# Kernel tuning notes

Hardware: AMD Instinct MI355X
Metric: run time of the kernel (lower is better)

Reference implementation:

```python
import jax, jax.numpy as jnp
import numpy as np
import math

N_SRC = 100000
N_DST0 = 30000
N_DST1 = 8000
E0 = 200000
E1 = 80000
H, D = 4, 64


def gat_conv(h_src, h_dst, src, dst, W, al, ar, b, n_dst):
    """DGL GATConv (allow_zero_in_degree=True): shared fc, LeakyReLU(0.2), edge softmax."""
    z_src = (h_src @ W).reshape(-1, H, D)              # [Ns,H,D]
    z_dst = (h_dst @ W).reshape(-1, H, D)              # [Nd,H,D]
    el = jnp.sum(z_src * al, axis=-1)                  # [Ns,H]
    er = jnp.sum(z_dst * ar, axis=-1)                  # [Nd,H]
    e = jax.nn.leaky_relu(el[src] + er[dst], 0.2)      # [E,H]
    emax = jax.ops.segment_max(e, dst, num_segments=n_dst)
    emax = jnp.where(jnp.isfinite(emax), emax, 0.0)
    ex = jnp.exp(e - emax[dst])
    denom = jax.ops.segment_sum(ex, dst, num_segments=n_dst)
    denom = jnp.where(denom > 0, denom, 1.0)
    alpha = ex / denom[dst]                            # [E,H]
    out = jax.ops.segment_sum(alpha[:, :, None] * z_src[src], dst, num_segments=n_dst)
    return out + b.reshape(1, H, D)                    # [Nd,H,D]


def attn_pool(feat):
    """Self attention over relation/head slots, then mean over slots (attention(f,f,f).mean(dim=1))."""
    d = feat.shape[-1]
    scores = jnp.einsum('nsd,ntd->nst', feat, feat) / math.sqrt(d)
    p = jax.nn.softmax(scores, axis=-1)
    out = jnp.einsum('nst,ntd->nsd', p, feat)
    return out.mean(axis=1)                            # [N,d]


def rgat_layer(xu, xi, eii, eiu, eui, W, al, ar, b, n_dst_u, n_dst_i):
    du, di = xu[:n_dst_u], xi[:n_dst_i]
    # sorted canonical etypes: ('item','ii','item') < ('item','iu','user') < ('user','ui','item')
    out_ii = gat_conv(xi, di, eii[0], eii[1], W[0], al[0], ar[0], b[0], n_dst_i)
    out_iu = gat_conv(xi, du, eiu[0], eiu[1], W[1], al[1], ar[1], b[1], n_dst_u)
    out_ui = gat_conv(xu, di, eui[0], eui[1], W[2], al[2], ar[2], b[2], n_dst_i)
    feat_u = out_iu                                    # [Nu, H, D]
    feat_i = jnp.concatenate([out_ii, out_ui], axis=1) # [Ni, 2H, D]
    hu = attn_pool(feat_u)
    hi = attn_pool(feat_i)
    return jnp.concatenate([du, hu], axis=1), jnp.concatenate([di, hi], axis=1)


def setup_inputs() -> dict:
    key = jax.random.key(0)
    ks = jax.random.split(key, 24)
    inp = {
        'x_user': jax.random.normal(ks[0], (N_SRC, 64), jnp.float32),
        'x_item': jax.random.normal(ks[1], (N_SRC, 64), jnp.float32),
        'e0_ii_src': jax.random.randint(ks[2], (E0,), 0, N_SRC, jnp.int32),
        'e0_ii_dst': jax.random.randint(ks[3], (E0,), 0, N_DST0, jnp.int32),
        'e0_iu_src': jax.random.randint(ks[4], (E0,), 0, N_SRC, jnp.int32),
        'e0_iu_dst': jax.random.randint(ks[5], (E0,), 0, N_DST0, jnp.int32),
        'e0_ui_src': jax.random.randint(ks[6], (E0,), 0, N_SRC, jnp.int32),
        'e0_ui_dst': jax.random.randint(ks[7], (E0,), 0, N_DST0, jnp.int32),
        'e1_ii_src': jax.random.randint(ks[8], (E1,), 0, N_DST0, jnp.int32),
        'e1_ii_dst': jax.random.randint(ks[9], (E1,), 0, N_DST1, jnp.int32),
        'e1_iu_src': jax.random.randint(ks[10], (E1,), 0, N_DST0, jnp.int32),
        'e1_iu_dst': jax.random.randint(ks[11], (E1,), 0, N_DST1, jnp.int32),
        'e1_ui_src': jax.random.randint(ks[12], (E1,), 0, N_DST0, jnp.int32),
        'e1_ui_dst': jax.random.randint(ks[13], (E1,), 0, N_DST1, jnp.int32),
        'W0': jax.random.normal(ks[14], (3, 64, H * D), jnp.float32) * 0.1,
        'al0': jax.random.normal(ks[15], (3, H, D), jnp.float32) * 0.1,
        'ar0': jax.random.normal(ks[16], (3, H, D), jnp.float32) * 0.1,
        'b0': jnp.zeros((3, H * D), jnp.float32),
        'W1': jax.random.normal(ks[17], (3, 128, H * D), jnp.float32) * 0.1,
        'al1': jax.random.normal(ks[18], (3, H, D), jnp.float32) * 0.1,
        'ar1': jax.random.normal(ks[19], (3, H, D), jnp.float32) * 0.1,
        'b1': jnp.zeros((3, H * D), jnp.float32),
    }
    return inp


def reference(x_user, x_item,
              e0_ii_src, e0_ii_dst, e0_iu_src, e0_iu_dst, e0_ui_src, e0_ui_dst,
              e1_ii_src, e1_ii_dst, e1_iu_src, e1_iu_dst, e1_ui_src, e1_ui_dst,
              W0, al0, ar0, b0, W1, al1, ar1, b1):
    xu, xi = rgat_layer(x_user, x_item,
                        (e0_ii_src, e0_ii_dst), (e0_iu_src, e0_iu_dst), (e0_ui_src, e0_ui_dst),
                        W0, al0, ar0, b0, N_DST0, N_DST0)
    xu, xi = rgat_layer(xu, xi,
                        (e1_ii_src, e1_ii_dst), (e1_iu_src, e1_iu_dst), (e1_ui_src, e1_ui_dst),
                        W1, al1, ar1, b1, N_DST1, N_DST1)
    return jnp.concatenate([xu, xi], axis=0)  # [2*N_DST1, 128+64]
```

## Files before the change

### kernel.cpp

```cpp
#include <hip/hip_runtime.h>

#define NSRC   100000
#define NDST0  30000
#define NDST1  8000
#define E0N    200000
#define E1N    80000
#define HD     256
#define DD     64
#define CAP    64

typedef short bf16x8 __attribute__((ext_vector_type(8)));
typedef float f32x4  __attribute__((ext_vector_type(4)));

static __device__ __forceinline__ unsigned short f2bf(float f) {
    unsigned u = __float_as_uint(f);
    u += 0x7fffu + ((u >> 16) & 1u);
    return (unsigned short)(u >> 16);
}
static __device__ __forceinline__ unsigned pack2(float a, float b) {
    return (unsigned)f2bf(a) | ((unsigned)f2bf(b) << 16);
}
static __device__ __forceinline__ void fma4(float4& a, float s, const float4& b) {
    a.x = fmaf(s, b.x, a.x); a.y = fmaf(s, b.y, a.y);
    a.z = fmaf(s, b.z, a.z); a.w = fmaf(s, b.w, a.w);
}
static __device__ __forceinline__ float dot4(const float4& a, const float4& b) {
    return fmaf(a.x, b.x, fmaf(a.y, b.y, fmaf(a.z, b.z, a.w * b.w)));
}
static __device__ __forceinline__ float4 ld_bf4(const unsigned short* p) {
    uint2 u = *reinterpret_cast<const uint2*>(p);
    float4 r;
    r.x = __uint_as_float(u.x << 16);
    r.y = __uint_as_float(u.x & 0xffff0000u);
    r.z = __uint_as_float(u.y << 16);
    r.w = __uint_as_float(u.y & 0xffff0000u);
    return r;
}
static __device__ __forceinline__ void red4(float4& a, int m) {
    a.x += __shfl_xor(a.x, m, 64);
    a.y += __shfl_xor(a.y, m, 64);
    a.z += __shfl_xor(a.z, m, 64);
    a.w += __shfl_xor(a.w, m, 64);
}

template<int K>
__global__ void k_wprep(const float* __restrict__ W, const float* __restrict__ al,
                        const float* __restrict__ ar, float* __restrict__ wl,
                        float* __restrict__ wr, unsigned short* __restrict__ Wt)
{
    constexpr int WLRB = (3 * K * 4) / 256;
    int bx = blockIdx.x;
    if (bx < WLRB) {
        int tid = bx * 256 + threadIdx.x;
        int r = tid / (K * 4);
        int rem = tid - r * K * 4;
        int k = rem >> 2, h = rem & 3;
        const float* wrow = W + (size_t)r * K * HD + (size_t)k * HD + h * DD;
        const float* a_l = al + r * HD + h * DD;
        const float* a_r = ar + r * HD + h * DD;
        float sl = 0.f, sr = 0.f;
        for (int d = 0; d < DD; ++d) {
            float w = wrow[d];
            sl = fmaf(w, a_l[d], sl);
            sr = fmaf(w, a_r[d], sr);
        }
        wl[r * 512 + k * 4 + h] = sl;
        wr[r * 512 + k * 4 + h] = sr;
    } else {
        int r = bx - WLRB;
        const float* Wr = W + (size_t)r * K * HD;
        unsigned short* Wtr = Wt + (size_t)r * 256 * K;
        int c = threadIdx.x;
        #pragma unroll 4
        for (int k = 0; k < K; k += 2) {
            float a = Wr[(size_t)k * HD + c];
            float b = Wr[(size_t)(k + 1) * HD + c];
            *reinterpret_cast<unsigned*>(Wtr + (size_t)c * K + k) = pack2(a, b);
        }
    }
}

template<int K, bool MIRROR>
__global__ __launch_bounds__(256) void k_prep_x2(const float* __restrict__ XA,
                                                 const float* __restrict__ XB,
                                                 int M, int nd, int bpr,
                                                 const float* __restrict__ wl3,
                                                 const float* __restrict__ wr3,
                                                 float* __restrict__ el3,
                                                 float* __restrict__ er3,
                                                 unsigned short* __restrict__ XbA,
                                                 unsigned short* __restrict__ XbB)
{
    int bx = blockIdx.x;
    const bool item = bx < bpr;
    int row = (item ? bx : bx - bpr) * 256 + threadIdx.x;
    if (row >= M) return;
    const float* X = item ? XA : XB;
    const float4* xv = reinterpret_cast<const float4*>(X + (size_t)row * K);

    if (MIRROR) {
        unsigned short* xbrow = (item ? XbA : XbB) + (size_t)row * K;
        #pragma unroll
        for (int c2 = 0; c2 < K / 8; ++c2) {
            float4 a = xv[2 * c2], b = xv[2 * c2 + 1];
            uint4 w;
            w.x = pack2(a.x, a.y); w.y = pack2(a.z, a.w);
            w.z = pack2(b.x, b.y); w.w = pack2(b.z, b.w);
            reinterpret_cast<uint4*>(xbrow)[c2] = w;
        }
    }

    const float4* wlAv = reinterpret_cast<const float4*>(item ? wl3 : wl3 + 1024);
    const float4* wlBv = reinterpret_cast<const float4*>(wl3 + 512);
    float4 aA = make_float4(0.f, 0.f, 0.f, 0.f), aB = aA;
    #pragma unroll
    for (int c = 0; c < K / 4; ++c) {
        float4 x4 = xv[c];
        fma4(aA, x4.x, wlAv[c * 4 + 0]); fma4(aA, x4.y, wlAv[c * 4 + 1]);
        fma4(aA, x4.z, wlAv[c * 4 + 2]); fma4(aA, x4.w, wlAv[c * 4 + 3]);
        if (item) {
            fma4(aB, x4.x, wlBv[c * 4 + 0]); fma4(aB, x4.y, wlBv[c * 4 + 1]);
            fma4(aB, x4.z, wlBv[c * 4 + 2]); fma4(aB, x4.w, wlBv[c * 4 + 3]);
        }
    }
    if (item) {
        *reinterpret_cast<float4*>(el3 + (size_t)row * 4) = aA;
        *reinterpret_cast<float4*>(el3 + (size_t)NSRC * 4 + (size_t)row * 4) = aB;
    } else {
        *reinterpret_cast<float4*>(el3 + (size_t)2 * NSRC * 4 + (size_t)row * 4) = aA;
    }
    if (row < nd) {
        const float4* wrAv = reinterpret_cast<const float4*>(item ? wr3 : wr3 + 512);
        const float4* wrBv = reinterpret_cast<const float4*>(wr3 + 1024);
        float4 rA = make_float4(0.f, 0.f, 0.f, 0.f), rB = rA;
        #pragma unroll
        for (int c = 0; c < K / 4; ++c) {
            float4 x4 = xv[c];
            fma4(rA, x4.x, wrAv[c * 4 + 0]); fma4(rA, x4.y, wrAv[c * 4 + 1]);
            fma4(rA, x4.z, wrAv[c * 4 + 2]); fma4(rA, x4.w, wrAv[c * 4 + 3]);
            if (item) {
                fma4(rB, x4.x, wrBv[c * 4 + 0]); fma4(rB, x4.y, wrBv[c * 4 + 1]);
                fma4(rB, x4.z, wrBv[c * 4 + 2]); fma4(rB, x4.w, wrBv[c * 4 + 3]);
            }
        }
        if (item) {
            *reinterpret_cast<float4*>(er3 + (size_t)row * 4) = rA;
            *reinterpret_cast<float4*>(er3 + (size_t)2 * NDST0 * 4 + (size_t)row * 4) = rB;
        } else {
            *reinterpret_cast<float4*>(er3 + (size_t)NDST0 * 4 + (size_t)row * 4) = rA;
        }
    }
}

__global__ void k_fill3(const int* __restrict__ ed0, const int* __restrict__ ed1,
                        const int* __restrict__ ed2, const int* __restrict__ es0,
                        const int* __restrict__ es1, const int* __restrict__ es2,
                        int* __restrict__ cnt, int* __restrict__ bsrc,
                        int E, int nd, int bpr)
{
    int bx = blockIdx.x;
    int r = (bx >= 2 * bpr) ? 2 : (bx >= bpr ? 1 : 0);
    int e = (bx - r * bpr) * 256 + threadIdx.x;
    if (e >= E) return;
    const int* ed = (r == 0) ? ed0 : (r == 1 ? ed1 : ed2);
    const int* es = (r == 0) ? es0 : (r == 1 ? es1 : es2);
    int d = ed[e];
    int c = atomicAdd(&cnt[(size_t)r * nd + d], 1);
    if (c < CAP) bsrc[((size_t)r * nd + d) * CAP + c] = es[e];
}

template<int K>
__global__ __launch_bounds__(256) void k_agg3(const int* __restrict__ cnt,
                                              const int* __restrict__ bsrc,
                                              const float* __restrict__ el3,
                                              const float* __restrict__ er3,
                                              const unsigned short* __restrict__ xsA,
                                              const unsigned short* __restrict__ xsB,
                                              unsigned short* __restrict__ aggX,
                                              int nd, int bpr)
{
    constexpr int NV = K / 64;
    int bx = blockIdx.x;
    int r = (bx >= 2 * bpr) ? 2 : (bx >= bpr ? 1 : 0);
    int wid = ((bx - r * bpr) * 256 + (int)threadIdx.x) >> 6;
    int lane = threadIdx.x & 63;
    if (wid >= nd) return;
    int q = lane & 15, g = lane >> 4;
    const float* el = el3 + (size_t)r * NSRC * 4;
    const unsigned short* xsrc = (r < 2) ? xsA : xsB;
    int c = cnt[(size_t)r * nd + wid]; if (c > CAP) c = CAP;
    const int* lst = bsrc + ((size_t)r * nd + wid) * CAP;
    float4 er4 = *reinterpret_cast<const float4*>(er3 + (size_t)r * NDST0 * 4 + (size_t)wid * 4);

    int s_own = 0;
    float4 ex_own = make_float4(0.f, 0.f, 0.f, 0.f);
    if (lane < c) {
        s_own = lst[lane];
        float4 e4 = *reinterpret_cast<const float4*>(el + (size_t)s_own * 4);
        e4.x += er4.x; e4.y += er4.y; e4.z += er4.z; e4.w += er4.w;
        e4.x = e4.x > 0.f ? e4.x : 0.2f * e4.x;
        e4.y = e4.y > 0.f ? e4.y : 0.2f * e4.y;
        e4.z = e4.z > 0.f ? e4.z : 0.2f * e4.z;
        e4.w = e4.w > 0.f ? e4.w : 0.2f * e4.w;
        ex_own.x = __expf(e4.x); ex_own.y = __expf(e4.y);
        ex_own.z = __expf(e4.z); ex_own.w = __expf(e4.w);
    }

    float4 acc[4][NV];
    #pragma unroll
    for (int h = 0; h < 4; ++h)
        #pragma unroll
        for (int v = 0; v < NV; ++v) acc[h][v] = make_float4(0.f, 0.f, 0.f, 0.f);
    float4 den = make_float4(0.f, 0.f, 0.f, 0.f);

    const int nt = (c + 3) >> 2;
    for (int t = 0; t < nt; ++t) {
        int i = g + 4 * t;
        int ilane = i & 63;
        int   s   = __shfl(s_own,    ilane, 64);
        float ex0 = __shfl(ex_own.x, ilane, 64);
        float ex1 = __shfl(ex_own.y, ilane, 64);
        float ex2 = __shfl(ex_own.z, ilane, 64);
        float ex3 = __shfl(ex_own.w, ilane, 64);
        if (i < c) {
            const unsigned short* xp = xsrc + (size_t)s * K + q * 4 * NV;
            #pragma unroll
            for (int v = 0; v < NV; ++v) {
                float4 x4 = ld_bf4(xp + v * 4);
                fma4(acc[0][v], ex0, x4);
                fma4(acc[1][v], ex1, x4);
                fma4(acc[2][v], ex2, x4);
                fma4(acc[3][v], ex3, x4);
            }
            den.x += ex0; den.y += ex1; den.z += ex2; den.w += ex3;
        }
    }
    #pragma unroll
    for (int m = 16; m < 64; m <<= 1) {
        #pragma unroll
        for (int h = 0; h < 4; ++h)
            #pragma unroll
            for (int v = 0; v < NV; ++v) red4(acc[h][v], m);
        red4(den, m);
    }
    float invh[4];
    invh[0] = den.x > 0.f ? 1.f / den.x : 0.f;
    invh[1] = den.y > 0.f ? 1.f / den.y : 0.f;
    invh[2] = den.z > 0.f ? 1.f / den.z : 0.f;
    invh[3] = den.w > 0.f ? 1.f / den.w : 0.f;
    #pragma unroll
    for (int h = 0; h < 4; ++h) {
        unsigned short* op = aggX + ((size_t)r * nd * 4 + (size_t)wid * 4 + h) * K + q * 4 * NV;
        if (NV == 1) {
            uint2 w;
            w.x = pack2(acc[h][0].x * invh[h], acc[h][0].y * invh[h]);
            w.y = pack2(acc[h][0].z * invh[h], acc[h][0].w * invh[h]);
            *reinterpret_cast<uint2*>(op) = w;
        } else {
            uint4 w;
            w.x = pack2(acc[h][0].x * invh[h], acc[h][0].y * invh[h]);
            w.y = pack2(acc[h][0].z * invh[h], acc[h][0].w * invh[h]);
            w.z = pack2(acc[h][1].x * invh[h], acc[h][1].y * invh[h]);
            w.w = pack2(acc[h][1].z * invh[h], acc[h][1].w * invh[h]);
            *reinterpret_cast<uint4*>(op) = w;
        }
    }
}

template<int K>
__global__ __launch_bounds__(256) void k_gemm3(const unsigned short* __restrict__ aggX,
                                               const unsigned short* __restrict__ Wt3,
                                               unsigned short* __restrict__ outb,
                                               int nd, int bpr)
{
    int bx = blockIdx.x;
    int r = (bx >= 2 * bpr) ? 2 : (bx >= bpr ? 1 : 0);
    const unsigned short* A  = aggX + (size_t)r * nd * 4 * K;
    const unsigned short* Wt = Wt3 + (size_t)r * 256 * K;
    unsigned short* ob = outb + (size_t)r * NDST0 * HD;
    const int lane = threadIdx.x & 63;
    const int wv = threadIdx.x >> 6;
    const int r0 = (bx - r * bpr) * 16;
    const int rr = lane & 15, kg = lane >> 4;
    f32x4 acc[4] = {{0.f,0.f,0.f,0.f},{0.f,0.f,0.f,0.f},{0.f,0.f,0.f,0.f},{0.f,0.f,0.f,0.f}};
    const unsigned short* ap = A + ((size_t)(r0 + rr) * 4 + wv) * K + kg * 8;
    #pragma unroll
    for (int kb = 0; kb < K; kb += 32) {
        bf16x8 a = *reinterpret_cast<const bf16x8*>(ap + kb);
        #pragma unroll
        for (int n = 0; n < 4; ++n) {
            const unsigned short* wp = Wt + (size_t)(wv * 64 + n * 16 + rr) * K + kb + kg * 8;
            bf16x8 b = *reinterpret_cast<const bf16x8*>(wp);
            acc[n] = __builtin_amdgcn_mfma_f32_16x16x32_bf16(a, b, acc[n], 0, 0, 0);
        }
    }
    #pragma unroll
    for (int n = 0; n < 4; ++n)
        #pragma unroll
        for (int i = 0; i < 4; ++i)
            ob[(size_t)(r0 + kg * 4 + i) * HD + wv * 64 + n * 16 + rr] = f2bf(acc[n][i]);
}

template<int S>
__global__ __launch_bounds__(256) void k_pool2(const unsigned short* __restrict__ srcA, const float* __restrict__ bA,
                                               const unsigned short* __restrict__ srcB, const float* __restrict__ bB,
                                               const float* __restrict__ base, int baseCols,
                                               float* __restrict__ dst, int pitch, int colOff, int n)
{
    int wid = (blockIdx.x * 256 + threadIdx.x) >> 6;
    int lane = threadIdx.x & 63;
    int node = wid * 4 + (lane >> 4);
    int q = lane & 15;
    if (node >= n) return;

    float4 f[S];
    #pragma unroll
    for (int s = 0; s < S; ++s) {
        const unsigned short* sp = (s < 4) ? (srcA + (size_t)node * HD + s * DD)
                                           : (srcB + (size_t)node * HD + (s - 4) * DD);
        const float* bp = (s < 4) ? (bA + s * DD) : (bB + (s - 4) * DD);
        float4 v = ld_bf4(sp + q * 4);
        float4 b = *reinterpret_cast<const float4*>(bp + q * 4);
        v.x += b.x; v.y += b.y; v.z += b.z; v.w += b.w;
        f[s] = v;
    }
    constexpr int NE = S * (S + 1) / 2;
    float gt[NE];
    {
        int idx = 0;
        #pragma unroll
        for (int s = 0; s < S; ++s)
            #pragma unroll
            for (int t = s; t < S; ++t)
                gt[idx++] = dot4(f[s], f[t]);
    }
    #pragma unroll
    for (int m = 1; m < 16; m <<= 1) {
        #pragma unroll
        for (int i = 0; i < NE; ++i) gt[i] += __shfl_xor(gt[i], m, 16);
    }
    auto Gv = [&](int s, int t) -> float {
        int a = s < t ? s : t, b2 = s < t ? t : s;
        return gt[a * S - a * (a - 1) / 2 + (b2 - a)];
    };
    float g[S];
    #pragma unroll
    for (int t = 0; t < S; ++t) g[t] = 0.f;
    #pragma unroll
    for (int s = 0; s < S; ++s) {
        float sc[S];
        float m = -1e30f;
        #pragma unroll
        for (int t = 0; t < S; ++t) { sc[t] = Gv(s, t) * 0.125f; m = sc[t] > m ? sc[t] : m; }
        float pe[S];
        float sum = 0.f;
        #pragma unroll
        for (int t = 0; t < S; ++t) { pe[t] = __expf(sc[t] - m); sum += pe[t]; }
        float inv = 1.f / sum;
        #pragma unroll
        for (int t = 0; t < S; ++t) g[t] += pe[t] * inv;
    }
    float4 o = make_float4(0.f, 0.f, 0.f, 0.f);
    #pragma unroll
    for (int t = 0; t < S; ++t) fma4(o, g[t], f[t]);
    const float is = 1.f / S;
    o.x *= is; o.y *= is; o.z *= is; o.w *= is;
    *reinterpret_cast<float4*>(dst + (size_t)node * pitch + colOff + q * 4) = o;
    for (int c = q * 4; c < baseCols; c += 64) {
        float4 v = *reinterpret_cast<const float4*>(base + (size_t)node * baseCols + c);
        *reinterpret_cast<float4*>(dst + (size_t)node * pitch + c) = v;
    }
}

extern "C" void kernel_launch(void* const* d_in, const int* in_sizes, int n_in,
                              void* d_out, int out_size, void* d_ws, size_t ws_size,
                              hipStream_t stream)
{
    const float* x_user = (const float*)d_in[0];
    const float* x_item = (const float*)d_in[1];
    const int* e_s[6] = { (const int*)d_in[2], (const int*)d_in[4], (const int*)d_in[6],
                          (const int*)d_in[8], (const int*)d_in[10], (const int*)d_in[12] };
    const int* e_d[6] = { (const int*)d_in[3], (const int*)d_in[5], (const int*)d_in[7],
                          (const int*)d_in[9], (const int*)d_in[11], (const int*)d_in[13] };
    const float* W0  = (const float*)d_in[14];
    const float* al0 = (const float*)d_in[15];
    const float* ar0 = (const float*)d_in[16];
    const float* b0  = (const float*)d_in[17];
    const float* W1  = (const float*)d_in[18];
    const float* al1 = (const float*)d_in[19];
    const float* ar1 = (const float*)d_in[20];
    const float* b1  = (const float*)d_in[21];
    float* out = (float*)d_out;
    (void)in_sizes; (void)n_in; (void)out_size; (void)ws_size;

    char* p = (char*)d_ws;
    auto take = [&](size_t bytes) { char* r = p; p += (bytes + 255) & ~(size_t)255; return r; };
    unsigned short* out3 = (unsigned short*)take((size_t)3 * NDST0 * HD * 2);
    float* xu1  = (float*)take((size_t)NDST0 * 128 * 4);
    float* xi1  = (float*)take((size_t)NDST0 * 128 * 4);
    unsigned short* xib  = (unsigned short*)take((size_t)NSRC * DD * 2);
    unsigned short* xub  = (unsigned short*)take((size_t)NSRC * DD * 2);
    unsigned short* xi1b = (unsigned short*)take((size_t)NDST0 * 128 * 2);
    unsigned short* xu1b = (unsigned short*)take((size_t)NDST0 * 128 * 2);
    unsigned short* aggX = (unsigned short*)take((size_t)3 * NDST0 * 4 * DD * 2);
    float* el3  = (float*)take((size_t)3 * NSRC * 4 * 4);
    float* er3  = (float*)take((size_t)3 * NDST0 * 4 * 4);
    int*   cntA = (int*)take((size_t)3 * NDST0 * 4);
    int*   cntB = (int*)take((size_t)3 * NDST1 * 4);
    int*   bsrcA = (int*)take((size_t)3 * NDST0 * CAP * 4);
    int*   bsrcB = (int*)take((size_t)3 * NDST1 * CAP * 4);
    unsigned short* Wt3 = (unsigned short*)take((size_t)3 * 256 * 128 * 2);
    float* wl3  = (float*)take((size_t)3 * 512 * 4);
    float* wr3  = (float*)take((size_t)3 * 512 * 4);

    unsigned short* out_ii = out3;
    unsigned short* out_iu = out3 + (size_t)NDST0 * HD;
    unsigned short* out_ui = out3 + (size_t)2 * NDST0 * HD;

    hipMemsetAsync(cntA, 0, (size_t)3 * NDST0 * 4, stream);
    hipMemsetAsync(cntB, 0, (size_t)3 * NDST1 * 4, stream);
    {
        const int bpr0 = (E0N + 255) / 256;
        k_fill3<<<3 * bpr0, 256, 0, stream>>>(e_d[0], e_d[1], e_d[2], e_s[0], e_s[1], e_s[2],
                                              cntA, bsrcA, E0N, NDST0, bpr0);
        const int bpr1 = (E1N + 255) / 256;
        k_fill3<<<3 * bpr1, 256, 0, stream>>>(e_d[3], e_d[4], e_d[5], e_s[3], e_s[4], e_s[5],
                                              cntB, bsrcB, E1N, NDST1, bpr1);
    }

    k_wprep<64><<<6, 256, 0, stream>>>(W0, al0, ar0, wl3, wr3, Wt3);
    {
        const int bpr = (NSRC + 255) / 256;
        k_prep_x2<64, true><<<2 * bpr, 256, 0, stream>>>(x_item, x_user, NSRC, NDST0, bpr,
                                                         wl3, wr3, el3, er3, xib, xub);
    }
    {
        const int bprA = (NDST0 + 3) / 4;
        k_agg3<64><<<3 * bprA, 256, 0, stream>>>(cntA, bsrcA, el3, er3, xib, xub,
                                                 aggX, NDST0, bprA);
        const int bprG = NDST0 / 16;
        k_gemm3<64><<<3 * bprG, 256, 0, stream>>>(aggX, Wt3, out3, NDST0, bprG);
    }
    k_pool2<4><<<NDST0 / 16, 256, 0, stream>>>(out_iu, b0 + 256, out_iu, b0 + 256,
                                               x_user, 64, xu1, 128, 64, NDST0);
    k_pool2<8><<<NDST0 / 16, 256, 0, stream>>>(out_ii, b0, out_ui, b0 + 512,
                                               x_item, 64, xi1, 128, 64, NDST0);

    k_wprep<128><<<9, 256, 0, stream>>>(W1, al1, ar1, wl3, wr3, Wt3);
    {
        const int bpr = (NDST0 + 255) / 256;
        k_prep_x2<128, true><<<2 * bpr, 256, 0, stream>>>(xi1, xu1, NDST0, NDST1, bpr,
                                                          wl3, wr3, el3, er3, xi1b, xu1b);
    }
    {
        const int bprA = (NDST1 + 3) / 4;
        k_agg3<128><<<3 * bprA, 256, 0, stream>>>(cntB, bsrcB, el3, er3, xi1b, xu1b,
                                                  aggX, NDST1, bprA);
        const int bprG = NDST1 / 16;
        k_gemm3<128><<<3 * bprG, 256, 0, stream>>>(aggX, Wt3, out3, NDST1, bprG);
    }
    k_pool2<4><<<NDST1 / 16, 256, 0, stream>>>(out_iu, b1 + 256, out_iu, b1 + 256,
                                               xu1, 128, out, 192, 128, NDST1);
    k_pool2<8><<<NDST1 / 16, 256, 0, stream>>>(out_ii, b1, out_ui, b1 + 512,
                                               xi1, 128, out + (size_t)NDST1 * 192, 192, 128, NDST1);
}
```

Before: 345.6 us.

## Gather fp32 source features directly and fuse setup kernels into one launch

```diff
diff --git a/kernel.cpp b/kernel.cpp
--- a/kernel.cpp
+++ b/kernel.cpp
@@ -36,60 +36,92 @@
     r.w = __uint_as_float(u.y & 0xffff0000u);
     return r;
 }
-static __device__ __forceinline__ void red4(float4& a, int m) {
-    a.x += __shfl_xor(a.x, m, 64);
-    a.y += __shfl_xor(a.y, m, 64);
-    a.z += __shfl_xor(a.z, m, 64);
-    a.w += __shfl_xor(a.w, m, 64);
+
+static __device__ void wlr_prep(const float* __restrict__ W, const float* __restrict__ al,
+                                const float* __restrict__ ar, float* __restrict__ wl,
+                                float* __restrict__ wr, int K, int tid)
+{
+    int r = tid / (K * 4);
+    int rem = tid - r * K * 4;
+    int k = rem >> 2, h = rem & 3;
+    const float* wrow = W + (size_t)r * K * HD + (size_t)k * HD + h * DD;
+    const float* a_l = al + r * HD + h * DD;
+    const float* a_r = ar + r * HD + h * DD;
+    float sl = 0.f, sr = 0.f;
+    for (int d = 0; d < DD; ++d) {
+        float w = wrow[d];
+        sl = fmaf(w, a_l[d], sl);
+        sr = fmaf(w, a_r[d], sr);
+    }
+    wl[r * 512 + k * 4 + h] = sl;
+    wr[r * 512 + k * 4 + h] = sr;
+}
+static __device__ void wt_prep(const float* __restrict__ W, unsigned short* __restrict__ Wt,
+                               int K, int r, int c)
+{
+    const float* Wr = W + (size_t)r * K * HD;
+    unsigned short* Wtr = Wt + (size_t)r * 256 * K;
+    for (int k = 0; k < K; k += 2) {
+        float a = Wr[(size_t)k * HD + c];
+        float b = Wr[(size_t)(k + 1) * HD + c];
+        *reinterpret_cast<unsigned*>(Wtr + (size_t)c * K + k) = pack2(a, b);
+    }
+}
+static __device__ void fill_one(const int* __restrict__ ed, const int* __restrict__ es,
+                                int* __restrict__ cnt, int* __restrict__ bsrc,
+                                int E, int nd, int r, int e)
+{
+    if (e >= E) return;
+    int d = ed[e];
+    int c = atomicAdd(&cnt[(size_t)r * nd + d], 1);
+    if (c < CAP) bsrc[((size_t)r * nd + d) * CAP + c] = es[e];
+}
+
+__global__ void k_setup(const int* ed0, const int* ed1, const int* ed2,
+                        const int* es0, const int* es1, const int* es2,
+                        const int* ed3, const int* ed4, const int* ed5,
+                        const int* es3, const int* es4, const int* es5,
+                        int* cntA, int* bsrcA, int* cntB, int* bsrcB,
+                        const float* W0, const float* al0, const float* ar0,
+                        const float* W1, const float* al1, const float* ar1,
+                        float* wlA, float* wrA, unsigned short* WtA,
+                        float* wlB, float* wrB, unsigned short* WtB,
+                        int bpr0, int bpr1)
+{
+    int bx = blockIdx.x;
+    int tid = threadIdx.x;
+    if (bx < 3 * bpr0) {
+        int r = (bx >= 2 * bpr0) ? 2 : (bx >= bpr0 ? 1 : 0);
+        int e = (bx - r * bpr0) * 256 + tid;
+        const int* ed = (r == 0) ? ed0 : (r == 1 ? ed1 : ed2);
+        const int* es = (r == 0) ? es0 : (r == 1 ? es1 : es2);
+        fill_one(ed, es, cntA, bsrcA, E0N, NDST0, r, e);
+        return;
+    }
+    bx -= 3 * bpr0;
+    if (bx < 3 * bpr1) {
+        int r = (bx >= 2 * bpr1) ? 2 : (bx >= bpr1 ? 1 : 0);
+        int e = (bx - r * bpr1) * 256 + tid;
+        const int* ed = (r == 0) ? ed3 : (r == 1 ? ed4 : ed5);
+        const int* es = (r == 0) ? es3 : (r == 1 ? es4 : es5);
+        fill_one(ed, es, cntB, bsrcB, E1N, NDST1, r, e);
+        return;
+    }
+    bx -= 3 * bpr1;
+    if (bx < 3)       wlr_prep(W0, al0, ar0, wlA, wrA, 64,  bx * 256 + tid);
+    else if (bx < 9)  wlr_prep(W1, al1, ar1, wlB, wrB, 128, (bx - 3) * 256 + tid);
+    else if (bx < 12) wt_prep(W0, WtA, 64,  bx - 9,  tid);
+    else              wt_prep(W1, WtB, 128, bx - 12, tid);
 }
 
 template<int K>
-__global__ void k_wprep(const float* __restrict__ W, const float* __restrict__ al,
-                        const float* __restrict__ ar, float* __restrict__ wl,
-                        float* __restrict__ wr, unsigned short* __restrict__ Wt)
-{
-    constexpr int WLRB = (3 * K * 4) / 256;
-    int bx = blockIdx.x;
-    if (bx < WLRB) {
-        int tid = bx * 256 + threadIdx.x;
-        int r = tid / (K * 4);
-        int rem = tid - r * K * 4;
-        int k = rem >> 2, h = rem & 3;
-        const float* wrow = W + (size_t)r * K * HD + (size_t)k * HD + h * DD;
-        const float* a_l = al + r * HD + h * DD;
-        const float* a_r = ar + r * HD + h * DD;
-        float sl = 0.f, sr = 0.f;
-        for (int d = 0; d < DD; ++d) {
-            float w = wrow[d];
-            sl = fmaf(w, a_l[d], sl);
-            sr = fmaf(w, a_r[d], sr);
-        }
-        wl[r * 512 + k * 4 + h] = sl;
-        wr[r * 512 + k * 4 + h] = sr;
-    } else {
-        int r = bx - WLRB;
-        const float* Wr = W + (size_t)r * K * HD;
-        unsigned short* Wtr = Wt + (size_t)r * 256 * K;
-        int c = threadIdx.x;
-        #pragma unroll 4
-        for (int k = 0; k < K; k += 2) {
-            float a = Wr[(size_t)k * HD + c];
-            float b = Wr[(size_t)(k + 1) * HD + c];
-            *reinterpret_cast<unsigned*>(Wtr + (size_t)c * K + k) = pack2(a, b);
-        }
-    }
-}
-
-template<int K, bool MIRROR>
 __global__ __launch_bounds__(256) void k_prep_x2(const float* __restrict__ XA,
                                                  const float* __restrict__ XB,
                                                  int M, int nd, int bpr,
                                                  const float* __restrict__ wl3,
                                                  const float* __restrict__ wr3,
                                                  float* __restrict__ el3,
-                                                 float* __restrict__ er3,
-                                                 unsigned short* __restrict__ XbA,
-                                                 unsigned short* __restrict__ XbB)
+                                                 float* __restrict__ er3)
 {
     int bx = blockIdx.x;
     const bool item = bx < bpr;
@@ -97,18 +129,6 @@
     if (row >= M) return;
     const float* X = item ? XA : XB;
     const float4* xv = reinterpret_cast<const float4*>(X + (size_t)row * K);
-
-    if (MIRROR) {
-        unsigned short* xbrow = (item ? XbA : XbB) + (size_t)row * K;
-        #pragma unroll
-        for (int c2 = 0; c2 < K / 8; ++c2) {
-            float4 a = xv[2 * c2], b = xv[2 * c2 + 1];
-            uint4 w;
-            w.x = pack2(a.x, a.y); w.y = pack2(a.z, a.w);
-            w.z = pack2(b.x, b.y); w.w = pack2(b.z, b.w);
-            reinterpret_cast<uint4*>(xbrow)[c2] = w;
-        }
-    }
 
     const float4* wlAv = reinterpret_cast<const float4*>(item ? wl3 : wl3 + 1024);
     const float4* wlBv = reinterpret_cast<const float4*>(wl3 + 512);
@@ -152,34 +172,18 @@
     }
 }
 
-__global__ void k_fill3(const int* __restrict__ ed0, const int* __restrict__ ed1,
-                        const int* __restrict__ ed2, const int* __restrict__ es0,
-                        const int* __restrict__ es1, const int* __restrict__ es2,
-                        int* __restrict__ cnt, int* __restrict__ bsrc,
-                        int E, int nd, int bpr)
-{
-    int bx = blockIdx.x;
-    int r = (bx >= 2 * bpr) ? 2 : (bx >= bpr ? 1 : 0);
-    int e = (bx - r * bpr) * 256 + threadIdx.x;
-    if (e >= E) return;
-    const int* ed = (r == 0) ? ed0 : (r == 1 ? ed1 : ed2);
-    const int* es = (r == 0) ? es0 : (r == 1 ? es1 : es2);
-    int d = ed[e];
-    int c = atomicAdd(&cnt[(size_t)r * nd + d], 1);
-    if (c < CAP) bsrc[((size_t)r * nd + d) * CAP + c] = es[e];
-}
-
 template<int K>
 __global__ __launch_bounds__(256) void k_agg3(const int* __restrict__ cnt,
                                               const int* __restrict__ bsrc,
                                               const float* __restrict__ el3,
                                               const float* __restrict__ er3,
-                                              const unsigned short* __restrict__ xsA,
-                                              const unsigned short* __restrict__ xsB,
+                                              const float* __restrict__ xsA,
+                                              const float* __restrict__ xsB,
                                               unsigned short* __restrict__ aggX,
                                               int nd, int bpr)
 {
     constexpr int NV = K / 64;
+    __shared__ float exs[256][4];
     int bx = blockIdx.x;
     int r = (bx >= 2 * bpr) ? 2 : (bx >= bpr ? 1 : 0);
     int wid = ((bx - r * bpr) * 256 + (int)threadIdx.x) >> 6;
@@ -187,7 +191,7 @@
     if (wid >= nd) return;
     int q = lane & 15, g = lane >> 4;
     const float* el = el3 + (size_t)r * NSRC * 4;
-    const unsigned short* xsrc = (r < 2) ? xsA : xsB;
+    const float* xsrc = (r < 2) ? xsA : xsB;
     int c = cnt[(size_t)r * nd + wid]; if (c > CAP) c = CAP;
     const int* lst = bsrc + ((size_t)r * nd + wid) * CAP;
     float4 er4 = *reinterpret_cast<const float4*>(er3 + (size_t)r * NDST0 * 4 + (size_t)wid * 4);
@@ -205,65 +209,36 @@
         ex_own.x = __expf(e4.x); ex_own.y = __expf(e4.y);
         ex_own.z = __expf(e4.z); ex_own.w = __expf(e4.w);
     }
-
-    float4 acc[4][NV];
-    #pragma unroll
-    for (int h = 0; h < 4; ++h)
-        #pragma unroll
-        for (int v = 0; v < NV; ++v) acc[h][v] = make_float4(0.f, 0.f, 0.f, 0.f);
-    float4 den = make_float4(0.f, 0.f, 0.f, 0.f);
-
-    const int nt = (c + 3) >> 2;
-    for (int t = 0; t < nt; ++t) {
-        int i = g + 4 * t;
-        int ilane = i & 63;
-        int   s   = __shfl(s_own,    ilane, 64);
-        float ex0 = __shfl(ex_own.x, ilane, 64);
-        float ex1 = __shfl(ex_own.y, ilane, 64);
-        float ex2 = __shfl(ex_own.z, ilane, 64);
-        float ex3 = __shfl(ex_own.w, ilane, 64);
-        if (i < c) {
-            const unsigned short* xp = xsrc + (size_t)s * K + q * 4 * NV;
-            #pragma unroll
-            for (int v = 0; v < NV; ++v) {
-                float4 x4 = ld_bf4(xp + v * 4);
-                fma4(acc[0][v], ex0, x4);
-                fma4(acc[1][v], ex1, x4);
-                fma4(acc[2][v], ex2, x4);
-                fma4(acc[3][v], ex3, x4);
-            }
-            den.x += ex0; den.y += ex1; den.z += ex2; den.w += ex3;
-        }
-    }
-    #pragma unroll
-    for (int m = 16; m < 64; m <<= 1) {
-        #pragma unroll
-        for (int h = 0; h < 4; ++h)
-            #pragma unroll
-            for (int v = 0; v < NV; ++v) red4(acc[h][v], m);
-        red4(den, m);
-    }
-    float invh[4];
-    invh[0] = den.x > 0.f ? 1.f / den.x : 0.f;
-    invh[1] = den.y > 0.f ? 1.f / den.y : 0.f;
-    invh[2] = den.z > 0.f ? 1.f / den.z : 0.f;
-    invh[3] = den.w > 0.f ? 1.f / den.w : 0.f;
-    #pragma unroll
-    for (int h = 0; h < 4; ++h) {
-        unsigned short* op = aggX + ((size_t)r * nd * 4 + (size_t)wid * 4 + h) * K + q * 4 * NV;
-        if (NV == 1) {
-            uint2 w;
-            w.x = pack2(acc[h][0].x * invh[h], acc[h][0].y * invh[h]);
-            w.y = pack2(acc[h][0].z * invh[h], acc[h][0].w * invh[h]);
-            *reinterpret_cast<uint2*>(op) = w;
-        } else {
-            uint4 w;
-            w.x = pack2(acc[h][0].x * invh[h], acc[h][0].y * invh[h]);
-            w.y = pack2(acc[h][0].z * invh[h], acc[h][0].w * invh[h]);
-            w.z = pack2(acc[h][1].x * invh[h], acc[h][1].y * invh[h]);
-            w.w = pack2(acc[h][1].z * invh[h], acc[h][1].w * invh[h]);
-            *reinterpret_cast<uint4*>(op) = w;
-        }
+    *reinterpret_cast<float4*>(&exs[threadIdx.x][0]) = ex_own;
+    const int wavebase = threadIdx.x & 192;
+
+    float4 acc[NV];
+    #pragma unroll
+    for (int v = 0; v < NV; ++v) acc[v] = make_float4(0.f, 0.f, 0.f, 0.f);
+    float den = 0.f;
+
+    for (int t = 0; t < c; ++t) {
+        int s = __shfl(s_own, t, 64);
+        float ex = exs[wavebase + t][g];
+        const float4* xp = reinterpret_cast<const float4*>(xsrc + (size_t)s * K) + q * NV;
+        #pragma unroll
+        for (int v = 0; v < NV; ++v) fma4(acc[v], ex, xp[v]);
+        den += ex;
+    }
+    float inv = den > 0.f ? 1.f / den : 0.f;
+    unsigned short* op = aggX + (((size_t)r * nd + wid) * 4 + g) * K + q * 4 * NV;
+    if (NV == 1) {
+        uint2 w;
+        w.x = pack2(acc[0].x * inv, acc[0].y * inv);
+        w.y = pack2(acc[0].z * inv, acc[0].w * inv);
+        *reinterpret_cast<uint2*>(op) = w;
+    } else {
+        uint4 w;
+        w.x = pack2(acc[0].x * inv, acc[0].y * inv);
+        w.y = pack2(acc[0].z * inv, acc[0].w * inv);
+        w.z = pack2(acc[1].x * inv, acc[1].y * inv);
+        w.w = pack2(acc[1].z * inv, acc[1].w * inv);
+        *reinterpret_cast<uint4*>(op) = w;
     }
 }
 
@@ -398,10 +373,6 @@
     unsigned short* out3 = (unsigned short*)take((size_t)3 * NDST0 * HD * 2);
     float* xu1  = (float*)take((size_t)NDST0 * 128 * 4);
     float* xi1  = (float*)take((size_t)NDST0 * 128 * 4);
-    unsigned short* xib  = (unsigned short*)take((size_t)NSRC * DD * 2);
-    unsigned short* xub  = (unsigned short*)take((size_t)NSRC * DD * 2);
-    unsigned short* xi1b = (unsigned short*)take((size_t)NDST0 * 128 * 2);
-    unsigned short* xu1b = (unsigned short*)take((size_t)NDST0 * 128 * 2);
     unsigned short* aggX = (unsigned short*)take((size_t)3 * NDST0 * 4 * DD * 2);
     float* el3  = (float*)take((size_t)3 * NSRC * 4 * 4);
     float* er3  = (float*)take((size_t)3 * NDST0 * 4 * 4);
@@ -409,55 +380,54 @@
     int*   cntB = (int*)take((size_t)3 * NDST1 * 4);
     int*   bsrcA = (int*)take((size_t)3 * NDST0 * CAP * 4);
     int*   bsrcB = (int*)take((size_t)3 * NDST1 * CAP * 4);
-    unsigned short* Wt3 = (unsigned short*)take((size_t)3 * 256 * 128 * 2);
-    float* wl3  = (float*)take((size_t)3 * 512 * 4);
-    float* wr3  = (float*)take((size_t)3 * 512 * 4);
+    unsigned short* WtA = (unsigned short*)take((size_t)3 * 256 * 64 * 2);
+    unsigned short* WtB = (unsigned short*)take((size_t)3 * 256 * 128 * 2);
+    float* wlA = (float*)take((size_t)3 * 512 * 4);
+    float* wrA = (float*)take((size_t)3 * 512 * 4);
+    float* wlB = (float*)take((size_t)3 * 512 * 4);
+    float* wrB = (float*)take((size_t)3 * 512 * 4);
 
     unsigned short* out_ii = out3;
     unsigned short* out_iu = out3 + (size_t)NDST0 * HD;
     unsigned short* out_ui = out3 + (size_t)2 * NDST0 * HD;
 
-    hipMemsetAsync(cntA, 0, (size_t)3 * NDST0 * 4, stream);
-    hipMemsetAsync(cntB, 0, (size_t)3 * NDST1 * 4, stream);
     {
-        const int bpr0 = (E0N + 255) / 256;
-        k_fill3<<<3 * bpr0, 256, 0, stream>>>(e_d[0], e_d[1], e_d[2], e_s[0], e_s[1], e_s[2],
-                                              cntA, bsrcA, E0N, NDST0, bpr0);
-        const int bpr1 = (E1N + 255) / 256;
-        k_fill3<<<3 * bpr1, 256, 0, stream>>>(e_d[3], e_d[4], e_d[5], e_s[3], e_s[4], e_s[5],
-                                              cntB, bsrcB, E1N, NDST1, bpr1);
-    }
-
-    k_wprep<64><<<6, 256, 0, stream>>>(W0, al0, ar0, wl3, wr3, Wt3);
+        size_t cntSpan = (size_t)((char*)cntB - (char*)cntA) + (size_t)3 * NDST1 * 4;
+        hipMemsetAsync(cntA, 0, cntSpan, stream);
+    }
+    const int bpr0 = (E0N + 255) / 256;
+    const int bpr1 = (E1N + 255) / 256;
+    k_setup<<<3 * bpr0 + 3 * bpr1 + 15, 256, 0, stream>>>(
+        e_d[0], e_d[1], e_d[2], e_s[0], e_s[1], e_s[2],
+        e_d[3], e_d[4], e_d[5], e_s[3], e_s[4], e_s[5],
+        cntA, bsrcA, cntB, bsrcB,
+        W0, al0, ar0, W1, al1, ar1,
+        wlA, wrA, WtA, wlB, wrB, WtB, bpr0, bpr1);
+
     {
         const int bpr = (NSRC + 255) / 256;
-        k_prep_x2<64, true><<<2 * bpr, 256, 0, stream>>>(x_item, x_user, NSRC, NDST0, bpr,
-                                                         wl3, wr3, el3, er3, xib, xub);
-    }
-    {
+        k_prep_x2<64><<<2 * bpr, 256, 0, stream>>>(x_item, x_user, NSRC, NDST0, bpr,
+                                                   wlA, wrA, el3, er3);
         const int bprA = (NDST0 + 3) / 4;
-        k_agg3<64><<<3 * bprA, 256, 0, stream>>>(cntA, bsrcA, el3, er3, xib, xub,
+        k_agg3<64><<<3 * bprA, 256, 0, stream>>>(cntA, bsrcA, el3, er3, x_item, x_user,
                                                  aggX, NDST0, bprA);
         const int bprG = NDST0 / 16;
-        k_gemm3<64><<<3 * bprG, 256, 0, stream>>>(aggX, Wt3, out3, NDST0, bprG);
+        k_gemm3<64><<<3 * bprG, 256, 0, stream>>>(aggX, WtA, out3, NDST0, bprG);
     }
     k_pool2<4><<<NDST0 / 16, 256, 0, stream>>>(out_iu, b0 + 256, out_iu, b0 + 256,
                                                x_user, 64, xu1, 128, 64, NDST0);
     k_pool2<8><<<NDST0 / 16, 256, 0, stream>>>(out_ii, b0, out_ui, b0 + 512,
                                                x_item, 64, xi1, 128, 64, NDST0);
 
-    k_wprep<128><<<9, 256, 0, stream>>>(W1, al1, ar1, wl3, wr3, Wt3);
     {
         const int bpr = (NDST0 + 255) / 256;
-        k_prep_x2<128, true><<<2 * bpr, 256, 0, stream>>>(xi1, xu1, NDST0, NDST1, bpr,
-                                                          wl3, wr3, el3, er3, xi1b, xu1b);
-    }
-    {
+        k_prep_x2<128><<<2 * bpr, 256, 0, stream>>>(xi1, xu1, NDST0, NDST1, bpr,
+                                                    wlB, wrB, el3, er3);
         const int bprA = (NDST1 + 3) / 4;
-        k_agg3<128><<<3 * bprA, 256, 0, stream>>>(cntB, bsrcB, el3, er3, xi1b, xu1b,
+        k_agg3<128><<<3 * bprA, 256, 0, stream>>>(cntB, bsrcB, el3, er3, xi1, xu1,
                                                   aggX, NDST1, bprA);
         const int bprG = NDST1 / 16;
-        k_gemm3<128><<<3 * bprG, 256, 0, stream>>>(aggX, Wt3, out3, NDST1, bprG);
+        k_gemm3<128><<<3 * bprG, 256, 0, stream>>>(aggX, WtB, out3, NDST1, bprG);
     }
     k_pool2<4><<<NDST1 / 16, 256, 0, stream>>>(out_iu, b1 + 256, out_iu, b1 + 256,
                                                xu1, 128, out, 192, 128, NDST1);
```

Measured after the change: 317.5 us. 1.09x faster.
